# Kernel tuning notes

Measured on AMD Instinct MI355X. Metric: run time of the kernel, lower is better.

The kernel has to match this reference:

```python
import jax, jax.numpy as jnp
import numpy as np

B, S, H = 1024, 16, 1024
N = 16384          # retrieved neighbors per user
L = 128            # num_labels


def setup_inputs() -> dict:
    key = jax.random.key(0)
    ks = jax.random.split(key, 6)
    features = jax.random.normal(ks[0], (B, S, H), dtype=jnp.float32)
    sims = jax.random.uniform(ks[1], (B, N), dtype=jnp.float32)
    labels = jax.random.randint(ks[2], (B, N), 0, L, dtype=jnp.int32)
    dense_w = jax.random.normal(ks[3], (H, H + L), dtype=jnp.float32) * 0.02
    dense_b = jnp.zeros((H,), dtype=jnp.float32)
    out_w = jax.random.normal(ks[4], (L, H), dtype=jnp.float32) * 0.02
    out_b = jnp.zeros((L,), dtype=jnp.float32)
    return {
        "features": features,
        "user_texts_similarities": sims,
        "user_texts_labels": labels,
        "dense_w": dense_w,
        "dense_b": dense_b,
        "out_w": out_w,
        "out_b": out_b,
    }


def _aggregate_labels(sims, labels):
    # mean over N of one_hot(labels) * sims  ->  scatter-add then divide.
    b, n = sims.shape
    agg = jnp.zeros((b, L), dtype=sims.dtype)
    rows = jnp.arange(b, dtype=jnp.int32)[:, None]  # [B,1] broadcast against [B,N]
    agg = agg.at[rows, labels].add(sims)
    return agg / n  # [B, L]


def reference(features, user_texts_similarities, user_texts_labels,
              dense_w, dense_b, out_w, out_b):
    # top_k=None, normalize_weights=False, feature_normalization='none', eval (dropout=id)
    agg = _aggregate_labels(user_texts_similarities, user_texts_labels)  # [B, L]
    cls = features[:, 0, :]                                              # [B, H]
    x = jnp.concatenate((cls, agg), axis=1)                              # [B, H+L]
    x = jnp.tanh(x @ dense_w.T + dense_b)                                # [B, H]
    return x @ out_w.T + out_b                                           # [B, L]
```

## Files before the change

kernel.cpp:

```cpp
#include <hip/hip_runtime.h>

#define B_DIM 1024
#define S_DIM 16
#define H_DIM 1024
#define N_DIM 16384
#define L_DIM 128
#define KX    (H_DIM + L_DIM)

typedef __bf16 bf16_8 __attribute__((ext_vector_type(8)));
typedef float  f32x4  __attribute__((ext_vector_type(4)));

__device__ __forceinline__ unsigned short f2bf(float f) {
    unsigned int u = __float_as_uint(f);
    u += 0x7fffu + ((u >> 16) & 1u);
    return (unsigned short)(u >> 16);
}

#define GLD16(gp, lp)                                                          \
    __builtin_amdgcn_global_load_lds(                                          \
        (const __attribute__((address_space(1))) void*)(gp),                   \
        (__attribute__((address_space(3))) void*)(lp), 16, 0, 0)

__global__ __launch_bounds__(64) void k_agg(
    const float* __restrict__ feats,
    const float* __restrict__ sims,
    const int*   __restrict__ labels,
    unsigned short* __restrict__ xin)
{
    __shared__ float bins[L_DIM * 64];
    const int bb = blockIdx.x;
    const int t  = threadIdx.x;

    #pragma unroll
    for (int i = 0; i < L_DIM; ++i) bins[i * 64 + t] = 0.f;
    __syncthreads();

    const float4* s4 = (const float4*)(sims   + (size_t)bb * N_DIM);
    const int4*   l4 = (const int4*)  (labels + (size_t)bb * N_DIM);

    float4 fs[2][4];
    int4   fl[2][4];

#define LOADB(slot, bt)                                                        \
    do {                                                                       \
        _Pragma("unroll")                                                      \
        for (int q = 0; q < 4; ++q) {                                          \
            fs[slot][q] = s4[((bt) * 4 + q) * 64 + t];                         \
            fl[slot][q] = l4[((bt) * 4 + q) * 64 + t];                         \
        }                                                                      \
    } while (0)

    LOADB(0, 0);
    LOADB(1, 1);
    #pragma unroll
    for (int bt = 0; bt < 16; ++bt) {
        const int sl = bt & 1;
        int   ad[16];
        float vv[16], rr[16];
        #pragma unroll
        for (int q = 0; q < 4; ++q) {
            const int*   lp = (const int*)  &fl[sl][q];
            const float* sp = (const float*)&fs[sl][q];
            #pragma unroll
            for (int k = 0; k < 4; ++k) {
                const int e   = q * 4 + k;
                const int i   = bt * 16 + e;
                const int col = (t + i) & 63;
                ad[e] = lp[k] * 64 + col;
                vv[e] = sp[k];
            }
        }
        #pragma unroll
        for (int e = 0; e < 16; ++e) rr[e] = bins[ad[e]];
        #pragma unroll
        for (int e = 0; e < 16; ++e) bins[ad[e]] = rr[e] + vv[e];
        if (bt + 2 < 16) LOADB(sl, bt + 2);
    }
    __syncthreads();

    unsigned short* xrow = xin + (size_t)bb * KX;
    const float4* c4 = (const float4*)(feats + (size_t)bb * (S_DIM * H_DIM));
    #pragma unroll
    for (int i = 0; i < 4; ++i) {
        float4 cv = c4[t + i * 64];
        ushort4 p;
        p.x = f2bf(cv.x); p.y = f2bf(cv.y); p.z = f2bf(cv.z); p.w = f2bf(cv.w);
        *(ushort4*)(xrow + (t + i * 64) * 4) = p;
    }

    #pragma unroll
    for (int pb = 0; pb < 2; ++pb) {
        const int l = pb * 64 + t;
        float a0 = 0.f, a1 = 0.f, a2 = 0.f, a3 = 0.f;
        #pragma unroll
        for (int i = 0; i < 64; i += 4) {
            a0 += bins[l * 64 + ((t + i)     & 63)];
            a1 += bins[l * 64 + ((t + i + 1) & 63)];
            a2 += bins[l * 64 + ((t + i + 2) & 63)];
            a3 += bins[l * 64 + ((t + i + 3) & 63)];
        }
        xrow[H_DIM + l] = f2bf((a0 + a1 + a2 + a3) * (1.0f / N_DIM));
    }
#undef LOADB
}

__global__ __launch_bounds__(256) void k_cvt(
    const float* __restrict__ w1, const float* __restrict__ w2,
    unsigned short* __restrict__ o1, unsigned short* __restrict__ o2,
    int n1v, int n2v)
{
    int idx = blockIdx.x * 256 + threadIdx.x;
    int stride = gridDim.x * 256;
    for (int i = idx; i < n1v + n2v; i += stride) {
        const float4* src; unsigned short* dst; int j;
        if (i < n1v) { src = (const float4*)w1; dst = o1; j = i; }
        else         { src = (const float4*)w2; dst = o2; j = i - n1v; }
        float4 v = src[j];
        ushort4 p;
        p.x = f2bf(v.x); p.y = f2bf(v.y); p.z = f2bf(v.z); p.w = f2bf(v.w);
        *(ushort4*)(dst + j * 4) = p;
    }
}

template <int EPI, int SWZ>
__global__ __launch_bounds__(256) void k_gemm(
    const unsigned short* __restrict__ A,
    const unsigned short* __restrict__ Bm,
    const float* __restrict__ bias,
    void* __restrict__ Cout,
    int M, int N, int K, int ldc)
{
    __shared__ __align__(16) unsigned short smA[3][128 * 64];
    __shared__ __align__(16) unsigned short smB[3][64 * 64];

    const int t    = threadIdx.x;
    const int lane = t & 63;
    const int w    = t >> 6;
    int m0, n0;
    if (SWZ) {
        const int d = blockIdx.x;
        n0 = (((d & 7) | ((d >> 6) << 3))) * 64;
        m0 = ((d >> 3) & 7) * 128;
    } else {
        m0 = blockIdx.y * 128;
        n0 = blockIdx.x * 64;
    }
    const int lr   = lane & 15;
    const int hi   = lane >> 4;
    const int sw   = lr & 7;

    int srcA[4], srcB[2];
    #pragma unroll
    for (int j = 0; j < 4; ++j) {
        int idx = t + j * 256;
        int row = idx >> 3;
        int g   = (idx & 7) ^ (row & 7);
        srcA[j] = row * K + g * 8;
    }
    #pragma unroll
    for (int j = 0; j < 2; ++j) {
        int idx = t + j * 256;
        int row = idx >> 3;
        int g   = (idx & 7) ^ (row & 7);
        srcB[j] = row * K + g * 8;
    }
    const size_t aBase = (size_t)m0 * K;
    const size_t bBase = (size_t)n0 * K;

    const int nt = K >> 6;
    f32x4 acc[2][4] = {};

#define STAGE(buf, k0_)                                                        \
    do {                                                                       \
        _Pragma("unroll")                                                      \
        for (int j = 0; j < 4; ++j)                                            \
            GLD16(A + aBase + (size_t)(srcA[j] + (k0_)),                       \
                  &smA[buf][(t + j * 256) * 8]);                               \
        _Pragma("unroll")                                                      \
        for (int j = 0; j < 2; ++j)                                            \
            GLD16(Bm + bBase + (size_t)(srcB[j] + (k0_)),                      \
                  &smB[buf][(t + j * 256) * 8]);                               \
    } while (0)

    STAGE(0, 0);
    if (nt > 1) STAGE(1, 64);

    int cur = 0;
    for (int ti = 0; ti < nt; ++ti) {
        int b2 = cur + 2; if (b2 >= 3) b2 -= 3;
        if (ti + 2 < nt) {
            STAGE(b2, (ti + 2) << 6);
            asm volatile("s_waitcnt vmcnt(12)" ::: "memory");
        } else if (ti + 1 < nt) {
            asm volatile("s_waitcnt vmcnt(6)" ::: "memory");
        } else {
            asm volatile("s_waitcnt vmcnt(0)" ::: "memory");
        }
        __builtin_amdgcn_s_barrier();
        asm volatile("" ::: "memory");

        const unsigned short* As = smA[cur];
        const unsigned short* Bs = smB[cur];
        #pragma unroll
        for (int ks = 0; ks < 2; ++ks) {
            const int ga = ((ks * 4 + hi) ^ sw) * 8;
            bf16_8 a0 = *(const bf16_8*)(As + (w * 32 +      lr) * 64 + ga);
            bf16_8 a1 = *(const bf16_8*)(As + (w * 32 + 16 + lr) * 64 + ga);
            bf16_8 b0 = *(const bf16_8*)(Bs + (      lr) * 64 + ga);
            bf16_8 b1 = *(const bf16_8*)(Bs + (16  + lr) * 64 + ga);
            bf16_8 b2v = *(const bf16_8*)(Bs + (32 + lr) * 64 + ga);
            bf16_8 b3 = *(const bf16_8*)(Bs + (48  + lr) * 64 + ga);
            acc[0][0] = __builtin_amdgcn_mfma_f32_16x16x32_bf16(a0, b0,  acc[0][0], 0, 0, 0);
            acc[1][0] = __builtin_amdgcn_mfma_f32_16x16x32_bf16(a1, b0,  acc[1][0], 0, 0, 0);
            acc[0][1] = __builtin_amdgcn_mfma_f32_16x16x32_bf16(a0, b1,  acc[0][1], 0, 0, 0);
            acc[1][1] = __builtin_amdgcn_mfma_f32_16x16x32_bf16(a1, b1,  acc[1][1], 0, 0, 0);
            acc[0][2] = __builtin_amdgcn_mfma_f32_16x16x32_bf16(a0, b2v, acc[0][2], 0, 0, 0);
            acc[1][2] = __builtin_amdgcn_mfma_f32_16x16x32_bf16(a1, b2v, acc[1][2], 0, 0, 0);
            acc[0][3] = __builtin_amdgcn_mfma_f32_16x16x32_bf16(a0, b3,  acc[0][3], 0, 0, 0);
            acc[1][3] = __builtin_amdgcn_mfma_f32_16x16x32_bf16(a1, b3,  acc[1][3], 0, 0, 0);
        }

        asm volatile("" ::: "memory");
        __builtin_amdgcn_s_barrier();
        cur = cur + 1; if (cur >= 3) cur = 0;
    }

    const int rbase = m0 + w * 32 + hi * 4;
    const int cbase = n0 + lr;
    #pragma unroll
    for (int i = 0; i < 2; ++i) {
        #pragma unroll
        for (int j = 0; j < 4; ++j) {
            int col = cbase + j * 16;
            float bv = bias[col];
            #pragma unroll
            for (int r = 0; r < 4; ++r) {
                int row = rbase + i * 16 + r;
                float v = acc[i][j][r] + bv;
                if (EPI == 0) {
                    v = tanhf(v);
                    ((unsigned short*)Cout)[(size_t)row * ldc + col] = f2bf(v);
                } else {
                    ((float*)Cout)[(size_t)row * ldc + col] = v;
                }
            }
        }
    }
#undef STAGE
}

extern "C" void kernel_launch(void* const* d_in, const int* in_sizes, int n_in,
                              void* d_out, int out_size, void* d_ws, size_t ws_size,
                              hipStream_t stream) {
    const float* feats   = (const float*)d_in[0];
    const float* sims    = (const float*)d_in[1];
    const int*   labels  = (const int*)  d_in[2];
    const float* dense_w = (const float*)d_in[3];
    const float* dense_b = (const float*)d_in[4];
    const float* out_w   = (const float*)d_in[5];
    const float* out_b   = (const float*)d_in[6];
    float* out = (float*)d_out;

    unsigned short* xin  = (unsigned short*)d_ws;
    unsigned short* wd   = xin  + (size_t)B_DIM * KX;
    unsigned short* wo   = wd   + (size_t)H_DIM * KX;
    unsigned short* xmid = wo   + (size_t)L_DIM * H_DIM;

    k_agg<<<B_DIM, 64, 0, stream>>>(feats, sims, labels, xin);

    int n1v = (H_DIM * KX) / 4;
    int n2v = (L_DIM * H_DIM) / 4;
    k_cvt<<<512, 256, 0, stream>>>(dense_w, out_w, wd, wo, n1v, n2v);

    k_gemm<0, 1><<<128, 256, 0, stream>>>(xin, wd, dense_b, (void*)xmid,
                                          B_DIM, H_DIM, KX, H_DIM);

    dim3 g2(L_DIM / 64, B_DIM / 128);
    k_gemm<1, 0><<<g2, 256, 0, stream>>>(xmid, wo, out_b, (void*)out,
                                         B_DIM, L_DIM, H_DIM, L_DIM);
}
```

Baseline: 226.6 us.

## Shrink GEMM tiles, add split-K with atomics, deepen prefetch pipelines

The GEMM tile shrinks from 128x64 to 64x64, so the first GEMM runs 256 blocks instead of 128 and the second uses split-K over 4 chunks with atomicAdd into an output pre-filled with the bias by a new k_fill kernel. The shared-memory pipeline grows to 4 stages, and the aggregation kernel's register prefetch grows from 2 to 4 batches. The goal is to fill more of the GPU's compute units and hide memory latency better. The costs are more register use, an extra kernel launch, atomic contention on the output, and run-to-run nondeterministic float summation order.

```diff
diff --git a/kernel.cpp b/kernel.cpp
--- a/kernel.cpp
+++ b/kernel.cpp
@@ -38,8 +38,8 @@
     const float4* s4 = (const float4*)(sims   + (size_t)bb * N_DIM);
     const int4*   l4 = (const int4*)  (labels + (size_t)bb * N_DIM);
 
-    float4 fs[2][4];
-    int4   fl[2][4];
+    float4 fs[4][4];
+    int4   fl[4][4];
 
 #define LOADB(slot, bt)                                                        \
     do {                                                                       \
@@ -52,9 +52,11 @@
 
     LOADB(0, 0);
     LOADB(1, 1);
+    LOADB(2, 2);
+    LOADB(3, 3);
     #pragma unroll
     for (int bt = 0; bt < 16; ++bt) {
-        const int sl = bt & 1;
+        const int sl = bt & 3;
         int   ad[16];
         float vv[16], rr[16];
         #pragma unroll
@@ -74,7 +76,7 @@
         for (int e = 0; e < 16; ++e) rr[e] = bins[ad[e]];
         #pragma unroll
         for (int e = 0; e < 16; ++e) bins[ad[e]] = rr[e] + vv[e];
-        if (bt + 2 < 16) LOADB(sl, bt + 2);
+        if (bt + 4 < 16) LOADB(sl, bt + 4);
     }
     __syncthreads();
 
@@ -122,77 +124,75 @@
     }
 }
 
-template <int EPI, int SWZ>
+__global__ __launch_bounds__(256) void k_fill(
+    float* __restrict__ out, const float* __restrict__ bias)
+{
+    int i4 = blockIdx.x * 256 + threadIdx.x;
+    int c  = (i4 * 4) & (L_DIM - 1);
+    float4 v = { bias[c], bias[c + 1], bias[c + 2], bias[c + 3] };
+    ((float4*)out)[i4] = v;
+}
+
+template <int EPI>
 __global__ __launch_bounds__(256) void k_gemm(
     const unsigned short* __restrict__ A,
     const unsigned short* __restrict__ Bm,
     const float* __restrict__ bias,
     void* __restrict__ Cout,
-    int M, int N, int K, int ldc)
-{
-    __shared__ __align__(16) unsigned short smA[3][128 * 64];
-    __shared__ __align__(16) unsigned short smB[3][64 * 64];
+    int LDK, int k_len, int ldc)
+{
+    __shared__ __align__(16) unsigned short smA[4][64 * 64];
+    __shared__ __align__(16) unsigned short smB[4][64 * 64];
 
     const int t    = threadIdx.x;
     const int lane = t & 63;
     const int w    = t >> 6;
-    int m0, n0;
-    if (SWZ) {
-        const int d = blockIdx.x;
-        n0 = (((d & 7) | ((d >> 6) << 3))) * 64;
-        m0 = ((d >> 3) & 7) * 128;
-    } else {
-        m0 = blockIdx.y * 128;
-        n0 = blockIdx.x * 64;
-    }
+    const int wm   = w >> 1, wn = w & 1;
+    const int m0   = blockIdx.y * 64;
+    const int n0   = blockIdx.x * 64;
+    const int kch  = blockIdx.z * k_len;
     const int lr   = lane & 15;
     const int hi   = lane >> 4;
     const int sw   = lr & 7;
 
-    int srcA[4], srcB[2];
-    #pragma unroll
-    for (int j = 0; j < 4; ++j) {
-        int idx = t + j * 256;
-        int row = idx >> 3;
-        int g   = (idx & 7) ^ (row & 7);
-        srcA[j] = row * K + g * 8;
-    }
+    int srcO[2];
     #pragma unroll
     for (int j = 0; j < 2; ++j) {
         int idx = t + j * 256;
         int row = idx >> 3;
         int g   = (idx & 7) ^ (row & 7);
-        srcB[j] = row * K + g * 8;
-    }
-    const size_t aBase = (size_t)m0 * K;
-    const size_t bBase = (size_t)n0 * K;
-
-    const int nt = K >> 6;
-    f32x4 acc[2][4] = {};
+        srcO[j] = row * LDK + g * 8;
+    }
+    const size_t aBase = (size_t)m0 * LDK + kch;
+    const size_t bBase = (size_t)n0 * LDK + kch;
+
+    const int nt = k_len >> 6;
+    f32x4 acc[2][2] = {};
 
 #define STAGE(buf, k0_)                                                        \
     do {                                                                       \
         _Pragma("unroll")                                                      \
-        for (int j = 0; j < 4; ++j)                                            \
-            GLD16(A + aBase + (size_t)(srcA[j] + (k0_)),                       \
+        for (int j = 0; j < 2; ++j) {                                          \
+            GLD16(A  + aBase + (size_t)(srcO[j] + (k0_)),                      \
                   &smA[buf][(t + j * 256) * 8]);                               \
-        _Pragma("unroll")                                                      \
-        for (int j = 0; j < 2; ++j)                                            \
-            GLD16(Bm + bBase + (size_t)(srcB[j] + (k0_)),                      \
+            GLD16(Bm + bBase + (size_t)(srcO[j] + (k0_)),                      \
                   &smB[buf][(t + j * 256) * 8]);                               \
+        }                                                                      \
     } while (0)
 
     STAGE(0, 0);
     if (nt > 1) STAGE(1, 64);
+    if (nt > 2) STAGE(2, 128);
 
     int cur = 0;
     for (int ti = 0; ti < nt; ++ti) {
-        int b2 = cur + 2; if (b2 >= 3) b2 -= 3;
-        if (ti + 2 < nt) {
-            STAGE(b2, (ti + 2) << 6);
+        if (ti + 3 < nt) {
+            STAGE((cur + 3) & 3, (ti + 3) << 6);
             asm volatile("s_waitcnt vmcnt(12)" ::: "memory");
+        } else if (ti + 2 < nt) {
+            asm volatile("s_waitcnt vmcnt(8)" ::: "memory");
         } else if (ti + 1 < nt) {
-            asm volatile("s_waitcnt vmcnt(6)" ::: "memory");
+            asm volatile("s_waitcnt vmcnt(4)" ::: "memory");
         } else {
             asm volatile("s_waitcnt vmcnt(0)" ::: "memory");
         }
@@ -204,35 +204,29 @@
         #pragma unroll
         for (int ks = 0; ks < 2; ++ks) {
             const int ga = ((ks * 4 + hi) ^ sw) * 8;
-            bf16_8 a0 = *(const bf16_8*)(As + (w * 32 +      lr) * 64 + ga);
-            bf16_8 a1 = *(const bf16_8*)(As + (w * 32 + 16 + lr) * 64 + ga);
-            bf16_8 b0 = *(const bf16_8*)(Bs + (      lr) * 64 + ga);
-            bf16_8 b1 = *(const bf16_8*)(Bs + (16  + lr) * 64 + ga);
-            bf16_8 b2v = *(const bf16_8*)(Bs + (32 + lr) * 64 + ga);
-            bf16_8 b3 = *(const bf16_8*)(Bs + (48  + lr) * 64 + ga);
-            acc[0][0] = __builtin_amdgcn_mfma_f32_16x16x32_bf16(a0, b0,  acc[0][0], 0, 0, 0);
-            acc[1][0] = __builtin_amdgcn_mfma_f32_16x16x32_bf16(a1, b0,  acc[1][0], 0, 0, 0);
-            acc[0][1] = __builtin_amdgcn_mfma_f32_16x16x32_bf16(a0, b1,  acc[0][1], 0, 0, 0);
-            acc[1][1] = __builtin_amdgcn_mfma_f32_16x16x32_bf16(a1, b1,  acc[1][1], 0, 0, 0);
-            acc[0][2] = __builtin_amdgcn_mfma_f32_16x16x32_bf16(a0, b2v, acc[0][2], 0, 0, 0);
-            acc[1][2] = __builtin_amdgcn_mfma_f32_16x16x32_bf16(a1, b2v, acc[1][2], 0, 0, 0);
-            acc[0][3] = __builtin_amdgcn_mfma_f32_16x16x32_bf16(a0, b3,  acc[0][3], 0, 0, 0);
-            acc[1][3] = __builtin_amdgcn_mfma_f32_16x16x32_bf16(a1, b3,  acc[1][3], 0, 0, 0);
+            bf16_8 a0 = *(const bf16_8*)(As + (wm * 32 +      lr) * 64 + ga);
+            bf16_8 a1 = *(const bf16_8*)(As + (wm * 32 + 16 + lr) * 64 + ga);
+            bf16_8 b0 = *(const bf16_8*)(Bs + (wn * 32 +      lr) * 64 + ga);
+            bf16_8 b1 = *(const bf16_8*)(Bs + (wn * 32 + 16 + lr) * 64 + ga);
+            acc[0][0] = __builtin_amdgcn_mfma_f32_16x16x32_bf16(a0, b0, acc[0][0], 0, 0, 0);
+            acc[1][0] = __builtin_amdgcn_mfma_f32_16x16x32_bf16(a1, b0, acc[1][0], 0, 0, 0);
+            acc[0][1] = __builtin_amdgcn_mfma_f32_16x16x32_bf16(a0, b1, acc[0][1], 0, 0, 0);
+            acc[1][1] = __builtin_amdgcn_mfma_f32_16x16x32_bf16(a1, b1, acc[1][1], 0, 0, 0);
         }
 
         asm volatile("" ::: "memory");
         __builtin_amdgcn_s_barrier();
-        cur = cur + 1; if (cur >= 3) cur = 0;
-    }
-
-    const int rbase = m0 + w * 32 + hi * 4;
-    const int cbase = n0 + lr;
+        cur = (cur + 1) & 3;
+    }
+
+    const int rbase = m0 + wm * 32 + hi * 4;
+    const int cbase = n0 + wn * 32 + lr;
     #pragma unroll
     for (int i = 0; i < 2; ++i) {
         #pragma unroll
-        for (int j = 0; j < 4; ++j) {
+        for (int j = 0; j < 2; ++j) {
             int col = cbase + j * 16;
-            float bv = bias[col];
+            float bv = (EPI < 2) ? bias[col] : 0.f;
             #pragma unroll
             for (int r = 0; r < 4; ++r) {
                 int row = rbase + i * 16 + r;
@@ -240,8 +234,10 @@
                 if (EPI == 0) {
                     v = tanhf(v);
                     ((unsigned short*)Cout)[(size_t)row * ldc + col] = f2bf(v);
+                } else if (EPI == 1) {
+                    ((float*)Cout)[(size_t)row * ldc + col] = v;
                 } else {
-                    ((float*)Cout)[(size_t)row * ldc + col] = v;
+                    atomicAdd(&((float*)Cout)[(size_t)row * ldc + col], v);
                 }
             }
         }
@@ -272,10 +268,13 @@
     int n2v = (L_DIM * H_DIM) / 4;
     k_cvt<<<512, 256, 0, stream>>>(dense_w, out_w, wd, wo, n1v, n2v);
 
-    k_gemm<0, 1><<<128, 256, 0, stream>>>(xin, wd, dense_b, (void*)xmid,
-                                          B_DIM, H_DIM, KX, H_DIM);
-
-    dim3 g2(L_DIM / 64, B_DIM / 128);
-    k_gemm<1, 0><<<g2, 256, 0, stream>>>(xmid, wo, out_b, (void*)out,
-                                         B_DIM, L_DIM, H_DIM, L_DIM);
-}
+    k_fill<<<(B_DIM * L_DIM / 4) / 256, 256, 0, stream>>>(out, out_b);
+
+    dim3 g1(H_DIM / 64, B_DIM / 64, 1);
+    k_gemm<0><<<g1, 256, 0, stream>>>(xin, wd, dense_b, (void*)xmid,
+                                      KX, KX, H_DIM);
+
+    dim3 g2(L_DIM / 64, B_DIM / 64, 4);
+    k_gemm<2><<<g2, 256, 0, stream>>>(xmid, wo, out_b, (void*)out,
+                                      H_DIM, H_DIM / 4, L_DIM);
+}
```

Measured after the change: 216.8 us. -4.4%, faster.
